# Kernel optimization log

Measured on AMD Instinct MI355X. Metric: run time of the kernel, lower is better.

The kernel has to match this reference:

```python
import jax, jax.numpy as jnp
from jax import lax
import numpy as np

BLANK = 0
PAD = 1
LABEL_SMOOTHING = 0.1
CE_SCALE = 1.0
TEMPERATURE = 1.0

B, T, U1, D, V = 8, 128, 33, 512, 4096  # U1 = U + 1


def setup_inputs() -> dict:
    key = jax.random.key(0)
    k0, k1, k2, k3, k4 = jax.random.split(key, 5)
    x = jax.random.normal(k0, (B, T, U1, D), dtype=jnp.float32)
    weight = jax.random.normal(k1, (V, D), dtype=jnp.float32) * 0.02
    bias = jnp.zeros((V,), dtype=jnp.float32)
    src_lengths = jax.random.randint(k2, (B,), T // 2, T + 1, dtype=jnp.int32)
    tgt_lengths = jax.random.randint(k3, (B,), U1 // 2, U1, dtype=jnp.int32)
    targets = jax.random.randint(k4, (B, U1 - 1), 2, V, dtype=jnp.int32)
    pos = jnp.arange(U1 - 1, dtype=jnp.int32)
    targets = jnp.where(pos[None, :] < tgt_lengths[:, None], targets, PAD)
    return {'x': x, 'weight': weight, 'bias': bias, 'targets': targets,
            'src_lengths': src_lengths, 'tgt_lengths': tgt_lengths}


def _rnnt_neglogp(blank_lp, emit_lp, src_lengths, tgt_lengths):
    """RNN-T forward DP. blank_lp: (B,T,U1) log P(blank); emit_lp: (B,T,U) log P(y_u).
    Returns per-utterance negative log-likelihood, shape (B,)."""
    Bn, Tn, U1n = blank_lp.shape
    # alpha at t=0: can only emit labels -> prefix-sum of emit log-probs
    alpha0 = jnp.concatenate(
        [jnp.zeros((Bn, 1), blank_lp.dtype), jnp.cumsum(emit_lp[:, 0, :], axis=1)], axis=1)

    def t_step(alpha_prev, xs):
        blank_prev, emit_t = xs  # (B,U1), (B,U)
        a = alpha_prev + blank_prev  # blank transition from t-1
        def u_step(c, xu):
            a_u, e_prev = xu  # each (B,)
            c = jnp.logaddexp(a_u, c + e_prev)  # emit transition from u-1 at same t
            return c, c
        _, rest = lax.scan(u_step, a[:, 0], (a[:, 1:].T, emit_t.T))  # rest: (U,B)
        alpha_t = jnp.concatenate([a[:, :1], rest.T], axis=1)
        return alpha_t, alpha_t

    xs = (jnp.swapaxes(blank_lp[:, :-1], 0, 1), jnp.swapaxes(emit_lp[:, 1:], 0, 1))
    _, alphas_rest = lax.scan(t_step, alpha0, xs)  # (T-1,B,U1)
    alphas = jnp.concatenate([alpha0[None], alphas_rest], axis=0)  # (T,B,U1)
    bidx = jnp.arange(Bn)
    alpha_last_t = alphas[src_lengths - 1, bidx]  # (B,U1)
    a_fin = jnp.take_along_axis(alpha_last_t, tgt_lengths[:, None], axis=1)[:, 0]
    b_fin = blank_lp[bidx, src_lengths - 1, tgt_lengths]  # final blank emission
    return -(a_fin + b_fin)


def reference(x, weight, bias, targets, src_lengths, tgt_lengths):
    Vn = weight.shape[0]
    # joint logits over full lattice: (B,T,U1,V)
    logits = (jnp.einsum('btud,vd->btuv', x, weight) + bias).astype(jnp.float32)
    lp = jax.nn.log_softmax(logits / TEMPERATURE, axis=-1)
    blank_lp = lp[..., BLANK]  # (B,T,U1)
    emit_lp = jnp.take_along_axis(lp[:, :, :-1, :], targets[:, None, :, None].astype(jnp.int32), axis=3)[..., 0]  # (B,T,U)
    loss_prob = jnp.sum(_rnnt_neglogp(blank_lp, emit_lp, src_lengths, tgt_lengths))
    loss_delay = jnp.zeros((), jnp.float32)  # delay_func == 'zero'
    # label-smoothed CE on last valid encoder frame
    last_h = jnp.take_along_axis(x, (src_lengths - 1)[:, None, None, None], axis=1)[:, 0]  # (B,U1,D)
    last_h = last_h[:, :-1]  # (B,U,D)
    ce_logits = (jnp.einsum('bud,vd->buv', last_h, weight) + bias).astype(jnp.float32)
    lprobs = jax.nn.log_softmax(ce_logits, axis=-1)
    nll = -jnp.take_along_axis(lprobs, targets[..., None], axis=-1)[..., 0]  # (B,U)
    smooth = -jnp.sum(lprobs, axis=-1)
    mask = (targets != PAD).astype(lprobs.dtype)
    eps_i = LABEL_SMOOTHING / (Vn - 1)
    loss_smoothed = jnp.sum(((1.0 - LABEL_SMOOTHING - eps_i) * nll + eps_i * smooth) * mask)
    total = loss_prob + loss_delay + CE_SCALE * loss_smoothed
    return total
```

## Files before the change

kernel.cpp:

```cpp
#include <hip/hip_runtime.h>
#include <hip/hip_bf16.h>
#include <math.h>

#define B_ 8
#define T_ 128
#define U1_ 33
#define D_ 512
#define V_ 4096
#define M_ (B_*T_*U1_)

#define BLANK_ 0
#define PAD_ 1

#define TM 128
#define TN 128
#define BK 32
#define NK (D_/BK)
#define GN (V_/TN)

typedef __attribute__((ext_vector_type(8))) short s8_t;
typedef __attribute__((ext_vector_type(4))) float fvec4;
typedef __attribute__((ext_vector_type(4))) unsigned short usvec4;
typedef unsigned short ushort_t;

__device__ __forceinline__ unsigned short f2bf(float f) {
    union { float f; unsigned u; } v; v.f = f;
    unsigned r = v.u + 0x7FFFu + ((v.u >> 16) & 1u);
    return (unsigned short)(r >> 16);
}

__device__ __forceinline__ void load_lds16(const ushort_t* g, ushort_t* l) {
    __builtin_amdgcn_global_load_lds(
        (const __attribute__((address_space(1))) unsigned int*)g,
        (__attribute__((address_space(3))) unsigned int*)l,
        16, 0, 0);
}

__global__ void convert_kernel(const float* __restrict__ x, const float* __restrict__ w,
                               ushort_t* __restrict__ xbf, ushort_t* __restrict__ wbf)
{
    int i = blockIdx.x * 256 + threadIdx.x;
    int stride = gridDim.x * 256;
    const int nx = (M_ * D_) / 4;
    const int nw = (V_ * D_) / 4;
    for (int j = i; j < nx; j += stride) {
        fvec4 v = ((const fvec4*)x)[j];
        usvec4 o = { f2bf(v.x), f2bf(v.y), f2bf(v.z), f2bf(v.w) };
        ((usvec4*)xbf)[j] = o;
    }
    for (int j = i; j < nw; j += stride) {
        fvec4 v = ((const fvec4*)w)[j];
        usvec4 o = { f2bf(v.x), f2bf(v.y), f2bf(v.z), f2bf(v.w) };
        ((usvec4*)wbf)[j] = o;
    }
}

__global__ __launch_bounds__(256, 3)
void gemm_fused(const ushort_t* __restrict__ xbf, const ushort_t* __restrict__ wbf,
                const float* __restrict__ bias, const int* __restrict__ targets,
                float* __restrict__ partial, float* __restrict__ blank_z,
                float* __restrict__ emit_z)
{
    __shared__ __align__(16) ushort_t As[2][TM * BK];
    __shared__ __align__(16) ushort_t Bs[2][TN * BK];
    __shared__ float ps[TM];
    __shared__ int tgt_s[TM];

    const int tid  = threadIdx.x;
    const int lane = tid & 63;
    const int wid  = tid >> 6;
    const int m0   = blockIdx.x * TM;
    const int n0   = blockIdx.y * TN;

    const int srow  = wid * 16 + (lane >> 2);
    const int skcol = (lane & 3) * 8;
    const ushort_t* agp = xbf + (size_t)(m0 + srow) * D_ + skcol;
    const ushort_t* bgp = wbf + (size_t)(n0 + srow) * D_ + skcol;
    const int lbase = (wid * 16) * BK;

    fvec4 acc[4][4];
#pragma unroll
    for (int i = 0; i < 4; i++)
#pragma unroll
        for (int j = 0; j < 4; j++) acc[i][j] = (fvec4)0.0f;

    const int wrow = (wid >> 1) * 64;
    const int wcol = (wid & 1) * 64;
    const int m15  = lane & 15;
    const int quad = lane >> 4;

    auto stage = [&](int buf, int ks) {
        const ushort_t* ag = agp + ks * BK;
        const ushort_t* bg = bgp + ks * BK;
        load_lds16(ag,            &As[buf][lbase]);
        load_lds16(ag + 64 * D_,  &As[buf][lbase + 64 * BK]);
        load_lds16(bg,            &Bs[buf][lbase]);
        load_lds16(bg + 64 * D_,  &Bs[buf][lbase + 64 * BK]);
    };

    stage(0, 0);
    __syncthreads();

    for (int ks = 0; ks < NK; ks++) {
        const int cur = ks & 1;
        if (ks + 1 < NK) stage(cur ^ 1, ks + 1);

        s8_t af[4], bf[4];
#pragma unroll
        for (int mi = 0; mi < 4; mi++)
            af[mi] = *(const s8_t*)&As[cur][(wrow + mi*16 + m15) * BK + quad * 8];
#pragma unroll
        for (int ni = 0; ni < 4; ni++)
            bf[ni] = *(const s8_t*)&Bs[cur][(wcol + ni*16 + m15) * BK + quad * 8];
#pragma unroll
        for (int mi = 0; mi < 4; mi++)
#pragma unroll
            for (int ni = 0; ni < 4; ni++)
                acc[mi][ni] = __builtin_amdgcn_mfma_f32_16x16x32_bf16(
                                  af[mi], bf[ni], acc[mi][ni], 0, 0, 0);
        __syncthreads();
    }

    if (tid < TM) {
        ps[tid] = 0.0f;
        int row = m0 + tid;
        int u = row % U1_;
        int b = row / (T_ * U1_);
        tgt_s[tid] = (u < U1_ - 1) ? targets[b * (U1_ - 1) + u] : -1;
    }
    __syncthreads();

    float bv[4];
#pragma unroll
    for (int ni = 0; ni < 4; ni++) bv[ni] = bias[n0 + wcol + ni*16 + m15];

    const bool blank_lane = (blockIdx.y == 0) && (wcol == 0) && (m15 == 0);

#pragma unroll
    for (int mi = 0; mi < 4; mi++) {
#pragma unroll
        for (int r = 0; r < 4; r++) {
            const int irow = wrow + mi*16 + quad*4 + r;
            float s = 0.0f;
#pragma unroll
            for (int ni = 0; ni < 4; ni++) {
                float z = acc[mi][ni][r] + bv[ni];
                s += __expf(z);
                int c = n0 + wcol + ni*16 + m15;
                if (tgt_s[irow] == c) emit_z[m0 + irow] = z;
            }
            if (blank_lane) blank_z[m0 + irow] = acc[mi][0][r] + bv[0];
            s += __shfl_xor(s, 1, 64);
            s += __shfl_xor(s, 2, 64);
            s += __shfl_xor(s, 4, 64);
            s += __shfl_xor(s, 8, 64);
            if (m15 == 0) atomicAdd(&ps[irow], s);
        }
    }
    __syncthreads();
    if (tid < TM)
        partial[(size_t)blockIdx.y * M_ + m0 + tid] = ps[tid];
}

__global__ void lse_combine(const float* __restrict__ partial,
                            const float* __restrict__ blank_z, const float* __restrict__ emit_z,
                            float* __restrict__ lse, float* __restrict__ blank_lp,
                            float* __restrict__ emit_lp)
{
    int r = blockIdx.x * 256 + threadIdx.x;
    float s = 0.0f;
#pragma unroll
    for (int j = 0; j < GN; j++) s += partial[(size_t)j * M_ + r];
    float l = __logf(s);
    lse[r]      = l;
    blank_lp[r] = blank_z[r] - l;
    emit_lp[r]  = emit_z[r] - l;
}

__global__ void wsum_kernel(const float* __restrict__ w, const float* __restrict__ bias,
                            float* __restrict__ w_sum)
{
    int t  = threadIdx.x;
    int v0 = blockIdx.x * 128;
    float s0 = 0.0f, s1 = 0.0f;
    for (int v = 0; v < 128; v++) {
        s0 += w[(size_t)(v0 + v) * D_ + t];
        s1 += w[(size_t)(v0 + v) * D_ + t + 256];
    }
    atomicAdd(&w_sum[t], s0);
    atomicAdd(&w_sum[t + 256], s1);
    if (t < 128) atomicAdd(&w_sum[512], bias[v0 + t]);
}

__global__ __launch_bounds__(256)
void dp_kernel(const float* __restrict__ blank_lp, const float* __restrict__ emit_lp,
               const int* __restrict__ src_lengths, const int* __restrict__ tgt_lengths,
               float* __restrict__ out)
{
    __shared__ float blp[T_ * U1_];
    __shared__ float elp[T_ * U1_];
    const int tid = threadIdx.x;
    const int b = blockIdx.x;
    for (int i = tid; i < T_ * U1_; i += 256) {
        blp[i] = blank_lp[b * T_ * U1_ + i];
        elp[i] = emit_lp[b * T_ * U1_ + i];
    }
    __syncthreads();
    if (tid >= 64) return;

    const int u = tid;
    const int sl = src_lengths[b], tl = tgt_lengths[b];

    float val = 0.0f;
    float afin = 0.0f;

    for (int d = 1; d <= (T_ - 1) + (U1_ - 1); d++) {
        int t = d - u;
        float up = __shfl_up(val, 1, 64);
        bool valid = (u < U1_) && (t >= 0) && (t < T_);
        if (valid) {
            if (t == 0) {
                val = up + elp[u - 1];
            } else if (u == 0) {
                val = val + blp[(t - 1) * U1_];
            } else {
                float a1 = val + blp[(t - 1) * U1_ + u];
                float a2 = up  + elp[t * U1_ + (u - 1)];
                float mx = fmaxf(a1, a2), mn = fminf(a1, a2);
                val = mx + log1pf(__expf(mn - mx));
            }
            if (t == sl - 1 && u == tl) afin = val;
        }
    }
#pragma unroll
    for (int off = 1; off < 64; off <<= 1) afin += __shfl_xor(afin, off, 64);
    if (u == 0) {
        float bfin = blp[(sl - 1) * U1_ + tl];
        atomicAdd(out, -(afin + bfin));
    }
}

__global__ __launch_bounds__(256)
void ce_kernel(const float* __restrict__ x, const int* __restrict__ targets,
               const int* __restrict__ src_lengths,
               const float* __restrict__ emit_z, const float* __restrict__ lse,
               const float* __restrict__ w_sum, float* __restrict__ out)
{
    int gw   = (blockIdx.x * 256 + threadIdx.x) >> 6;
    int lane = threadIdx.x & 63;
    int b = gw >> 5;
    int u = gw & 31;
    int sl  = src_lengths[b];
    int tgt = targets[b * (U1_ - 1) + u];
    int row = (b * T_ + sl - 1) * U1_ + u;

    const fvec4* xr  = (const fvec4*)(x + (size_t)row * D_);
    const fvec4* ws4 = (const fvec4*)w_sum;
    float s = 0.0f;
#pragma unroll
    for (int j = 0; j < 2; j++) {
        fvec4 xv = xr[lane * 2 + j], wv = ws4[lane * 2 + j];
        s += xv.x * wv.x + xv.y * wv.y + xv.z * wv.z + xv.w * wv.w;
    }
#pragma unroll
    for (int off = 1; off < 64; off <<= 1) s += __shfl_xor(s, off, 64);

    if (lane == 0 && tgt != PAD_) {
        float zsum = s + w_sum[512];
        float l = lse[row];
        float nll = l - emit_z[row];
        float smooth = (float)V_ * l - zsum;
        const float eps_i = 0.1f / (float)(V_ - 1);
        float contrib = (1.0f - 0.1f - eps_i) * nll + eps_i * smooth;
        atomicAdd(out, contrib);
    }
}

extern "C" void kernel_launch(void* const* d_in, const int* in_sizes, int n_in,
                              void* d_out, int out_size, void* d_ws, size_t ws_size,
                              hipStream_t stream)
{
    const float* x           = (const float*)d_in[0];
    const float* w           = (const float*)d_in[1];
    const float* bias        = (const float*)d_in[2];
    const int*   targets     = (const int*)d_in[3];
    const int*   src_lengths = (const int*)d_in[4];
    const int*   tgt_lengths = (const int*)d_in[5];
    float* out = (float*)d_out;

    char* p = (char*)d_ws;
    ushort_t* xbf = (ushort_t*)p;              p += (size_t)M_ * D_ * sizeof(ushort_t);
    ushort_t* wbf = (ushort_t*)p;              p += (size_t)V_ * D_ * sizeof(ushort_t);
    float* partial  = (float*)p;               p += (size_t)GN * M_ * sizeof(float);
    float* lse      = (float*)p;               p += (size_t)M_ * sizeof(float);
    float* blank_z  = (float*)p;               p += (size_t)M_ * sizeof(float);
    float* emit_z   = (float*)p;               p += (size_t)M_ * sizeof(float);
    float* blank_lp = (float*)p;               p += (size_t)M_ * sizeof(float);
    float* emit_lp  = (float*)p;               p += (size_t)M_ * sizeof(float);
    float* w_sum    = (float*)p;               p += 513 * sizeof(float);

    hipMemsetAsync(out, 0, sizeof(float), stream);
    hipMemsetAsync(w_sum, 0, 513 * sizeof(float), stream);

    convert_kernel<<<4096, 256, 0, stream>>>(x, w, xbf, wbf);
    gemm_fused<<<dim3(M_/TM, V_/TN), 256, 0, stream>>>(xbf, wbf, bias, targets,
                                                       partial, blank_z, emit_z);
    lse_combine<<<M_/256, 256, 0, stream>>>(partial, blank_z, emit_z, lse, blank_lp, emit_lp);
    wsum_kernel<<<32, 256, 0, stream>>>(w, bias, w_sum);
    dp_kernel<<<B_, 256, 0, stream>>>(blank_lp, emit_lp, src_lengths, tgt_lengths, out);
    ce_kernel<<<64, 256, 0, stream>>>(x, targets, src_lengths, emit_z, lse, w_sum, out);
}
```

Baseline: 394.8 us.

## Switch GEMM to scaled FP8 MFMA and fold CE into LSE combine

Inputs and weights are now converted to FP8 (weights pre-scaled by 64, undone through MFMA block scales), and the GEMM uses the 16x16x128 f8f6f4 scaled MFMA with a 128-byte K tile and XOR-swizzled LDS. The GEMM also accumulates per-row logit sums, which lets the CE smoothing term be computed in lse_combine and removes the wsum and ce kernels. The DP kernel now derives log-probs from lse on load, and its LDS reads are hoisted out of the branch with clamped indices. FP8 halves GEMM input bytes and doubles MFMA throughput compared with bf16, at a notable cost in precision.

```diff
diff --git a/kernel.cpp b/kernel.cpp
--- a/kernel.cpp
+++ b/kernel.cpp
@@ -1,6 +1,7 @@
 #include <hip/hip_runtime.h>
 #include <hip/hip_bf16.h>
 #include <math.h>
+#include <stdint.h>
 
 #define B_ 8
 #define T_ 128
@@ -14,56 +15,58 @@
 
 #define TM 128
 #define TN 128
-#define BK 32
-#define NK (D_/BK)
+#define BKB 128
+#define NK (D_/BKB)
 #define GN (V_/TN)
 
-typedef __attribute__((ext_vector_type(8))) short s8_t;
 typedef __attribute__((ext_vector_type(4))) float fvec4;
-typedef __attribute__((ext_vector_type(4))) unsigned short usvec4;
-typedef unsigned short ushort_t;
-
-__device__ __forceinline__ unsigned short f2bf(float f) {
-    union { float f; unsigned u; } v; v.f = f;
-    unsigned r = v.u + 0x7FFFu + ((v.u >> 16) & 1u);
-    return (unsigned short)(r >> 16);
-}
-
-__device__ __forceinline__ void load_lds16(const ushort_t* g, ushort_t* l) {
+typedef __attribute__((ext_vector_type(8))) int   i8v;
+typedef __attribute__((ext_vector_type(4))) int   i4v;
+
+#define SCALE_A 0x7F7F7F7Fu
+#define SCALE_B 0x79797979u
+
+__device__ __forceinline__ void load_lds16(const uint8_t* g, uint8_t* l) {
     __builtin_amdgcn_global_load_lds(
         (const __attribute__((address_space(1))) unsigned int*)g,
-        (__attribute__((address_space(3))) unsigned int*)l,
-        16, 0, 0);
+        (__attribute__((address_space(3))) unsigned int*)l, 16, 0, 0);
+}
+
+__device__ __forceinline__ unsigned pack4_fp8(fvec4 v) {
+    int r = __builtin_amdgcn_cvt_pk_fp8_f32(v.x, v.y, 0, false);
+    r = __builtin_amdgcn_cvt_pk_fp8_f32(v.z, v.w, r, true);
+    return (unsigned)r;
 }
 
 __global__ void convert_kernel(const float* __restrict__ x, const float* __restrict__ w,
-                               ushort_t* __restrict__ xbf, ushort_t* __restrict__ wbf)
+                               uint8_t* __restrict__ xf8, uint8_t* __restrict__ wf8)
 {
     int i = blockIdx.x * 256 + threadIdx.x;
     int stride = gridDim.x * 256;
-    const int nx = (M_ * D_) / 4;
-    const int nw = (V_ * D_) / 4;
+    const int nx = (M_ * D_) / 16;
+    const int nw = (V_ * D_) / 16;
     for (int j = i; j < nx; j += stride) {
-        fvec4 v = ((const fvec4*)x)[j];
-        usvec4 o = { f2bf(v.x), f2bf(v.y), f2bf(v.z), f2bf(v.w) };
-        ((usvec4*)xbf)[j] = o;
+        const fvec4* p = (const fvec4*)x + (size_t)j * 4;
+        uint4 o = { pack4_fp8(p[0]), pack4_fp8(p[1]), pack4_fp8(p[2]), pack4_fp8(p[3]) };
+        ((uint4*)xf8)[j] = o;
     }
     for (int j = i; j < nw; j += stride) {
-        fvec4 v = ((const fvec4*)w)[j];
-        usvec4 o = { f2bf(v.x), f2bf(v.y), f2bf(v.z), f2bf(v.w) };
-        ((usvec4*)wbf)[j] = o;
-    }
-}
-
-__global__ __launch_bounds__(256, 3)
-void gemm_fused(const ushort_t* __restrict__ xbf, const ushort_t* __restrict__ wbf,
+        const fvec4* p = (const fvec4*)w + (size_t)j * 4;
+        fvec4 v0 = p[0]*64.0f, v1 = p[1]*64.0f, v2 = p[2]*64.0f, v3 = p[3]*64.0f;
+        uint4 o = { pack4_fp8(v0), pack4_fp8(v1), pack4_fp8(v2), pack4_fp8(v3) };
+        ((uint4*)wf8)[j] = o;
+    }
+}
+
+__global__ __launch_bounds__(256, 2)
+void gemm_fused(const uint8_t* __restrict__ xf8, const uint8_t* __restrict__ wf8,
                 const float* __restrict__ bias, const int* __restrict__ targets,
-                float* __restrict__ partial, float* __restrict__ blank_z,
-                float* __restrict__ emit_z)
-{
-    __shared__ __align__(16) ushort_t As[2][TM * BK];
-    __shared__ __align__(16) ushort_t Bs[2][TN * BK];
-    __shared__ float ps[TM];
+                float* __restrict__ partial_e, float* __restrict__ partial_z,
+                float* __restrict__ blank_z, float* __restrict__ emit_z)
+{
+    __shared__ __align__(16) uint8_t As[2][TM * BKB];
+    __shared__ __align__(16) uint8_t Bs[2][TN * BKB];
+    __shared__ float ps[TM], pz[TM];
     __shared__ int tgt_s[TM];
 
     const int tid  = threadIdx.x;
@@ -72,11 +75,10 @@
     const int m0   = blockIdx.x * TM;
     const int n0   = blockIdx.y * TN;
 
-    const int srow  = wid * 16 + (lane >> 2);
-    const int skcol = (lane & 3) * 8;
-    const ushort_t* agp = xbf + (size_t)(m0 + srow) * D_ + skcol;
-    const ushort_t* bgp = wbf + (size_t)(n0 + srow) * D_ + skcol;
-    const int lbase = (wid * 16) * BK;
+    const int srow = wid * 32 + (lane >> 3);
+    const int schk = (lane & 7) ^ ((lane >> 3) & 7);
+    const uint8_t* agp = xf8 + (size_t)(m0 + srow) * D_ + schk * 16;
+    const uint8_t* bgp = wf8 + (size_t)(n0 + srow) * D_ + schk * 16;
 
     fvec4 acc[4][4];
 #pragma unroll
@@ -90,39 +92,55 @@
     const int quad = lane >> 4;
 
     auto stage = [&](int buf, int ks) {
-        const ushort_t* ag = agp + ks * BK;
-        const ushort_t* bg = bgp + ks * BK;
-        load_lds16(ag,            &As[buf][lbase]);
-        load_lds16(ag + 64 * D_,  &As[buf][lbase + 64 * BK]);
-        load_lds16(bg,            &Bs[buf][lbase]);
-        load_lds16(bg + 64 * D_,  &Bs[buf][lbase + 64 * BK]);
+        const uint8_t* ag = agp + ks * BKB;
+        const uint8_t* bg = bgp + ks * BKB;
+#pragma unroll
+        for (int j = 0; j < 4; j++) {
+            load_lds16(ag + j * 8 * D_, &As[buf][(wid * 32 + j * 8) * BKB]);
+            load_lds16(bg + j * 8 * D_, &Bs[buf][(wid * 32 + j * 8) * BKB]);
+        }
     };
 
     stage(0, 0);
     __syncthreads();
+
+    const int e   = m15 & 7;
+    const int c0b = (((quad << 1) ^ e) << 4);
 
     for (int ks = 0; ks < NK; ks++) {
         const int cur = ks & 1;
         if (ks + 1 < NK) stage(cur ^ 1, ks + 1);
 
-        s8_t af[4], bf[4];
+        i8v fa[4], fb[4];
+#pragma unroll
+        for (int mi = 0; mi < 4; mi++) {
+            int base = (wrow + mi * 16 + m15) << 7;
+            union { i4v h[2]; i8v w; } u;
+            u.h[0] = *(const i4v*)&As[cur][base + c0b];
+            u.h[1] = *(const i4v*)&As[cur][base + (c0b ^ 16)];
+            fa[mi] = u.w;
+        }
+#pragma unroll
+        for (int ni = 0; ni < 4; ni++) {
+            int base = (wcol + ni * 16 + m15) << 7;
+            union { i4v h[2]; i8v w; } u;
+            u.h[0] = *(const i4v*)&Bs[cur][base + c0b];
+            u.h[1] = *(const i4v*)&Bs[cur][base + (c0b ^ 16)];
+            fb[ni] = u.w;
+        }
 #pragma unroll
         for (int mi = 0; mi < 4; mi++)
-            af[mi] = *(const s8_t*)&As[cur][(wrow + mi*16 + m15) * BK + quad * 8];
-#pragma unroll
-        for (int ni = 0; ni < 4; ni++)
-            bf[ni] = *(const s8_t*)&Bs[cur][(wcol + ni*16 + m15) * BK + quad * 8];
-#pragma unroll
-        for (int mi = 0; mi < 4; mi++)
 #pragma unroll
             for (int ni = 0; ni < 4; ni++)
-                acc[mi][ni] = __builtin_amdgcn_mfma_f32_16x16x32_bf16(
-                                  af[mi], bf[ni], acc[mi][ni], 0, 0, 0);
+                acc[mi][ni] = __builtin_amdgcn_mfma_scale_f32_16x16x128_f8f6f4(
+                                  fa[mi], fb[ni], acc[mi][ni],
+                                  0, 0,
+                                  0, SCALE_A, 0, SCALE_B);
         __syncthreads();
     }
 
     if (tid < TM) {
-        ps[tid] = 0.0f;
+        ps[tid] = 0.0f; pz[tid] = 0.0f;
         int row = m0 + tid;
         int u = row % U1_;
         int b = row / (T_ * U1_);
@@ -132,7 +150,7 @@
 
     float bv[4];
 #pragma unroll
-    for (int ni = 0; ni < 4; ni++) bv[ni] = bias[n0 + wcol + ni*16 + m15];
+    for (int ni = 0; ni < 4; ni++) bv[ni] = bias[n0 + wcol + ni * 16 + m15];
 
     const bool blank_lane = (blockIdx.y == 0) && (wcol == 0) && (m15 == 0);
 
@@ -140,75 +158,81 @@
     for (int mi = 0; mi < 4; mi++) {
 #pragma unroll
         for (int r = 0; r < 4; r++) {
-            const int irow = wrow + mi*16 + quad*4 + r;
-            float s = 0.0f;
+            const int irow = wrow + mi * 16 + quad * 4 + r;
+            float se = 0.0f, sz = 0.0f;
 #pragma unroll
             for (int ni = 0; ni < 4; ni++) {
                 float z = acc[mi][ni][r] + bv[ni];
-                s += __expf(z);
-                int c = n0 + wcol + ni*16 + m15;
+                se += __expf(z);
+                sz += z;
+                int c = n0 + wcol + ni * 16 + m15;
                 if (tgt_s[irow] == c) emit_z[m0 + irow] = z;
             }
             if (blank_lane) blank_z[m0 + irow] = acc[mi][0][r] + bv[0];
-            s += __shfl_xor(s, 1, 64);
-            s += __shfl_xor(s, 2, 64);
-            s += __shfl_xor(s, 4, 64);
-            s += __shfl_xor(s, 8, 64);
-            if (m15 == 0) atomicAdd(&ps[irow], s);
+            se += __shfl_xor(se, 1, 64); sz += __shfl_xor(sz, 1, 64);
+            se += __shfl_xor(se, 2, 64); sz += __shfl_xor(sz, 2, 64);
+            se += __shfl_xor(se, 4, 64); sz += __shfl_xor(sz, 4, 64);
+            se += __shfl_xor(se, 8, 64); sz += __shfl_xor(sz, 8, 64);
+            if (m15 == 0) { atomicAdd(&ps[irow], se); atomicAdd(&pz[irow], sz); }
         }
     }
     __syncthreads();
-    if (tid < TM)
-        partial[(size_t)blockIdx.y * M_ + m0 + tid] = ps[tid];
-}
-
-__global__ void lse_combine(const float* __restrict__ partial,
-                            const float* __restrict__ blank_z, const float* __restrict__ emit_z,
-                            float* __restrict__ lse, float* __restrict__ blank_lp,
-                            float* __restrict__ emit_lp)
+    if (tid < TM) {
+        partial_e[(size_t)blockIdx.y * M_ + m0 + tid] = ps[tid];
+        partial_z[(size_t)blockIdx.y * M_ + m0 + tid] = pz[tid];
+    }
+}
+
+__global__ void lse_combine(const float* __restrict__ partial_e, const float* __restrict__ partial_z,
+                            const float* __restrict__ emit_z, const int* __restrict__ targets,
+                            const int* __restrict__ src_lengths,
+                            float* __restrict__ lse, float* __restrict__ out)
 {
     int r = blockIdx.x * 256 + threadIdx.x;
-    float s = 0.0f;
-#pragma unroll
-    for (int j = 0; j < GN; j++) s += partial[(size_t)j * M_ + r];
-    float l = __logf(s);
-    lse[r]      = l;
-    blank_lp[r] = blank_z[r] - l;
-    emit_lp[r]  = emit_z[r] - l;
-}
-
-__global__ void wsum_kernel(const float* __restrict__ w, const float* __restrict__ bias,
-                            float* __restrict__ w_sum)
-{
-    int t  = threadIdx.x;
-    int v0 = blockIdx.x * 128;
-    float s0 = 0.0f, s1 = 0.0f;
-    for (int v = 0; v < 128; v++) {
-        s0 += w[(size_t)(v0 + v) * D_ + t];
-        s1 += w[(size_t)(v0 + v) * D_ + t + 256];
-    }
-    atomicAdd(&w_sum[t], s0);
-    atomicAdd(&w_sum[t + 256], s1);
-    if (t < 128) atomicAdd(&w_sum[512], bias[v0 + t]);
+    float se = 0.0f, sz = 0.0f;
+#pragma unroll
+    for (int j = 0; j < GN; j++) {
+        se += partial_e[(size_t)j * M_ + r];
+        sz += partial_z[(size_t)j * M_ + r];
+    }
+    float l = __logf(se);
+    lse[r] = l;
+
+    int b   = r / (T_ * U1_);
+    int rem = r % (T_ * U1_);
+    int t   = rem / U1_;
+    int u   = rem % U1_;
+    if (u < U1_ - 1 && t == src_lengths[b] - 1) {
+        int tgt = targets[b * (U1_ - 1) + u];
+        if (tgt != PAD_) {
+            float nll    = l - emit_z[r];
+            float smooth = (float)V_ * l - sz;
+            const float eps_i = 0.1f / (float)(V_ - 1);
+            atomicAdd(out, (1.0f - 0.1f - eps_i) * nll + eps_i * smooth);
+        }
+    }
 }
 
 __global__ __launch_bounds__(256)
-void dp_kernel(const float* __restrict__ blank_lp, const float* __restrict__ emit_lp,
-               const int* __restrict__ src_lengths, const int* __restrict__ tgt_lengths,
-               float* __restrict__ out)
+void dp_kernel(const float* __restrict__ blank_z, const float* __restrict__ emit_z,
+               const float* __restrict__ lse, const int* __restrict__ src_lengths,
+               const int* __restrict__ tgt_lengths, float* __restrict__ out)
 {
     __shared__ float blp[T_ * U1_];
     __shared__ float elp[T_ * U1_];
     const int tid = threadIdx.x;
     const int b = blockIdx.x;
     for (int i = tid; i < T_ * U1_; i += 256) {
-        blp[i] = blank_lp[b * T_ * U1_ + i];
-        elp[i] = emit_lp[b * T_ * U1_ + i];
+        int g = b * T_ * U1_ + i;
+        float l = lse[g];
+        blp[i] = blank_z[g] - l;
+        elp[i] = emit_z[g] - l;
     }
     __syncthreads();
     if (tid >= 64) return;
 
     const int u = tid;
+    const int ua = (u < U1_) ? u : U1_ - 1;
     const int sl = src_lengths[b], tl = tgt_lengths[b];
 
     float val = 0.0f;
@@ -216,16 +240,20 @@
 
     for (int d = 1; d <= (T_ - 1) + (U1_ - 1); d++) {
         int t = d - u;
+        int tb = t - 1; tb = tb < 0 ? 0 : (tb > T_ - 1 ? T_ - 1 : tb);
+        int tc = t < 0 ? 0 : (t > T_ - 1 ? T_ - 1 : t);
+        float blv = blp[tb * U1_ + ua];
+        float elv = elp[tc * U1_ + (ua > 0 ? ua - 1 : 0)];
         float up = __shfl_up(val, 1, 64);
         bool valid = (u < U1_) && (t >= 0) && (t < T_);
         if (valid) {
             if (t == 0) {
-                val = up + elp[u - 1];
+                val = up + elv;
             } else if (u == 0) {
-                val = val + blp[(t - 1) * U1_];
+                val = val + blv;
             } else {
-                float a1 = val + blp[(t - 1) * U1_ + u];
-                float a2 = up  + elp[t * U1_ + (u - 1)];
+                float a1 = val + blv;
+                float a2 = up + elv;
                 float mx = fmaxf(a1, a2), mn = fminf(a1, a2);
                 val = mx + log1pf(__expf(mn - mx));
             }
@@ -237,42 +265,6 @@
     if (u == 0) {
         float bfin = blp[(sl - 1) * U1_ + tl];
         atomicAdd(out, -(afin + bfin));
-    }
-}
-
-__global__ __launch_bounds__(256)
-void ce_kernel(const float* __restrict__ x, const int* __restrict__ targets,
-               const int* __restrict__ src_lengths,
-               const float* __restrict__ emit_z, const float* __restrict__ lse,
-               const float* __restrict__ w_sum, float* __restrict__ out)
-{
-    int gw   = (blockIdx.x * 256 + threadIdx.x) >> 6;
-    int lane = threadIdx.x & 63;
-    int b = gw >> 5;
-    int u = gw & 31;
-    int sl  = src_lengths[b];
-    int tgt = targets[b * (U1_ - 1) + u];
-    int row = (b * T_ + sl - 1) * U1_ + u;
-
-    const fvec4* xr  = (const fvec4*)(x + (size_t)row * D_);
-    const fvec4* ws4 = (const fvec4*)w_sum;
-    float s = 0.0f;
-#pragma unroll
-    for (int j = 0; j < 2; j++) {
-        fvec4 xv = xr[lane * 2 + j], wv = ws4[lane * 2 + j];
-        s += xv.x * wv.x + xv.y * wv.y + xv.z * wv.z + xv.w * wv.w;
-    }
-#pragma unroll
-    for (int off = 1; off < 64; off <<= 1) s += __shfl_xor(s, off, 64);
-
-    if (lane == 0 && tgt != PAD_) {
-        float zsum = s + w_sum[512];
-        float l = lse[row];
-        float nll = l - emit_z[row];
-        float smooth = (float)V_ * l - zsum;
-        const float eps_i = 0.1f / (float)(V_ - 1);
-        float contrib = (1.0f - 0.1f - eps_i) * nll + eps_i * smooth;
-        atomicAdd(out, contrib);
     }
 }
 
@@ -289,24 +281,20 @@
     float* out = (float*)d_out;
 
     char* p = (char*)d_ws;
-    ushort_t* xbf = (ushort_t*)p;              p += (size_t)M_ * D_ * sizeof(ushort_t);
-    ushort_t* wbf = (ushort_t*)p;              p += (size_t)V_ * D_ * sizeof(ushort_t);
-    float* partial  = (float*)p;               p += (size_t)GN * M_ * sizeof(float);
-    float* lse      = (float*)p;               p += (size_t)M_ * sizeof(float);
-    float* blank_z  = (float*)p;               p += (size_t)M_ * sizeof(float);
-    float* emit_z   = (float*)p;               p += (size_t)M_ * sizeof(float);
-    float* blank_lp = (float*)p;               p += (size_t)M_ * sizeof(float);
-    float* emit_lp  = (float*)p;               p += (size_t)M_ * sizeof(float);
-    float* w_sum    = (float*)p;               p += 513 * sizeof(float);
+    uint8_t* xf8 = (uint8_t*)p;     p += (size_t)M_ * D_;
+    uint8_t* wf8 = (uint8_t*)p;     p += (size_t)V_ * D_;
+    float* partial_e = (float*)p;   p += (size_t)GN * M_ * sizeof(float);
+    float* partial_z = (float*)p;   p += (size_t)GN * M_ * sizeof(float);
+    float* lse       = (float*)p;   p += (size_t)M_ * sizeof(float);
+    float* blank_z   = (float*)p;   p += (size_t)M_ * sizeof(float);
+    float* emit_z    = (float*)p;   p += (size_t)M_ * sizeof(float);
 
     hipMemsetAsync(out, 0, sizeof(float), stream);
-    hipMemsetAsync(w_sum, 0, 513 * sizeof(float), stream);
-
-    convert_kernel<<<4096, 256, 0, stream>>>(x, w, xbf, wbf);
-    gemm_fused<<<dim3(M_/TM, V_/TN), 256, 0, stream>>>(xbf, wbf, bias, targets,
-                                                       partial, blank_z, emit_z);
-    lse_combine<<<M_/256, 256, 0, stream>>>(partial, blank_z, emit_z, lse, blank_lp, emit_lp);
-    wsum_kernel<<<32, 256, 0, stream>>>(w, bias, w_sum);
-    dp_kernel<<<B_, 256, 0, stream>>>(blank_lp, emit_lp, src_lengths, tgt_lengths, out);
-    ce_kernel<<<64, 256, 0, stream>>>(x, targets, src_lengths, emit_z, lse, w_sum, out);
-}
+
+    convert_kernel<<<1536, 256, 0, stream>>>(x, w, xf8, wf8);
+    gemm_fused<<<dim3(M_/TM, V_/TN), 256, 0, stream>>>(xf8, wf8, bias, targets,
+                                                       partial_e, partial_z, blank_z, emit_z);
+    lse_combine<<<M_/256, 256, 0, stream>>>(partial_e, partial_z, emit_z, targets,
+                                            src_lengths, lse, out);
+    dp_kernel<<<B_, 256, 0, stream>>>(blank_z, emit_z, lse, src_lengths, tgt_lengths, out);
+}
```

Result: faster. 364.7 us (-7.6%).
